# Optimization experiments

Hardware: AMD Instinct MI355X
Metric: run time of the kernel (lower is better)

The kernel has to match this reference:

```python
import jax, jax.numpy as jnp
import numpy as np

B, C, H, W = 64, 256, 32, 32
K, D = 1024, 256
COMMIT = 0.25
DECAY = 0.99
EPS = 1e-05


def setup_inputs() -> dict:
    key = jax.random.key(0)
    k1, k2, k3 = jax.random.split(key, 3)
    return {
        "inputs": jax.random.normal(k1, (B, C, H, W), dtype=jnp.float32),
        "embedding": jax.random.normal(k2, (K, D), dtype=jnp.float32),
        "ema_cluster_size": jnp.zeros((K,), dtype=jnp.float32),
        "ema_w": jax.random.normal(k3, (K, D), dtype=jnp.float32),
    }


def reference(inputs, embedding, ema_cluster_size, ema_w):
    # NCHW -> NHWC, flatten to [N, D]
    x = jnp.transpose(inputs, (0, 2, 3, 1))  # [B,H,W,D]
    in_shape = x.shape
    flat = x.reshape(-1, D)  # [N, D]

    dist = (jnp.sum(flat * flat, axis=1, keepdims=True)
            + jnp.sum(embedding * embedding, axis=1)
            - 2.0 * jnp.matmul(flat, embedding.T))
    idx = jnp.argmin(dist, axis=1)  # [N] int
    encodings = jax.nn.one_hot(idx, K, dtype=flat.dtype)  # [N, K]

    quantized = jnp.matmul(encodings, embedding).reshape(in_shape)  # [B,H,W,D]

    # EMA updates (training branch)
    cluster = ema_cluster_size * DECAY + (1.0 - DECAY) * jnp.sum(encodings, axis=0)
    n = jnp.sum(cluster)
    cluster = (cluster + EPS) / (n + K * EPS) * n
    dw = jnp.matmul(encodings.T, flat)  # [K, D]
    new_ema_w = ema_w * DECAY + (1.0 - DECAY) * dw
    new_embedding = new_ema_w / cluster[:, None]

    # commitment loss (quantized detached)
    e_latent_loss = jnp.mean((jax.lax.stop_gradient(quantized) - x) ** 2)
    loss = COMMIT * e_latent_loss

    # straight-through estimator
    quantized_st = x + jax.lax.stop_gradient(quantized - x)

    avg_probs = jnp.mean(encodings, axis=0)
    vq_entropy = -jnp.sum(avg_probs * jnp.log(avg_probs + 1e-10))

    out = jnp.transpose(quantized_st, (0, 3, 1, 2))  # back to NCHW
    return out, loss, vq_entropy, encodings, cluster, new_ema_w, new_embedding
```

## Files before the change

kernel.cpp:

```cpp
#include <hip/hip_runtime.h>

#define B_    64
#define C_    256
#define H_    32
#define W_    32
#define K_    1024
#define D_    256
#define HW_   1024
#define N_    65536
#define NELEM 16777216
#define DECAY_ 0.99f
#define OMD_   0.01f
#define EPS_   1e-5f
#define TAU_   0.05f

#define OFF_LOSS    16777216
#define OFF_ENT     16777217
#define OFF_ENC     16777218
#define OFF_CLUSTER 83886082
#define OFF_NEWW    83887106
#define OFF_NEWEMB  84149250

#define OFF_XHI     (OFF_ENC + 2)
#define OFF_XLO     (OFF_XHI + 8388608)
#define OFF_EHI     (OFF_XLO + 8388608)
#define OFF_ELO     (OFF_EHI + 131072)
#define OFF_SORT2   (OFF_ELO + 131072)
#define ZTAIL_ABS   33884168
#define ZTAIL_F4    12500478
#define ZHEAD_F4    4276737

typedef __attribute__((ext_vector_type(8)))  short short8;
typedef __attribute__((ext_vector_type(16))) float floatx16;

__device__ __forceinline__ unsigned short f2bf(float f) {
    unsigned u = __float_as_uint(f);
    return (unsigned short)((u + 0x7fffu + ((u >> 16) & 1u)) >> 16);
}
__device__ __forceinline__ float bf2f(unsigned short h) {
    return __uint_as_float(((unsigned)h) << 16);
}

__global__ __launch_bounds__(64) void k_prep_e(const float* __restrict__ emb,
                                               unsigned short* __restrict__ ehi,
                                               unsigned short* __restrict__ elo,
                                               float* __restrict__ enorm) {
    const int k = blockIdx.x;
    const int t = threadIdx.x;
    float4 v = ((const float4*)(emb + (size_t)k * D_))[t];
    float s = v.x * v.x + v.y * v.y + v.z * v.z + v.w * v.w;
    ushort4 hi, lo;
    {
        float f[4] = {v.x, v.y, v.z, v.w};
        unsigned short h[4], l[4];
        #pragma unroll
        for (int j = 0; j < 4; ++j) {
            h[j] = f2bf(f[j]);
            l[j] = f2bf(f[j] - bf2f(h[j]));
        }
        hi = make_ushort4(h[0], h[1], h[2], h[3]);
        lo = make_ushort4(l[0], l[1], l[2], l[3]);
    }
    size_t o = ((size_t)(k >> 5) << 13) + ((size_t)(t >> 2) << 9)
             + (((size_t)(t >> 1) & 1) << 8) + ((size_t)(k & 31) << 3) + ((t & 1) << 2);
    *(ushort4*)(ehi + o) = hi;
    *(ushort4*)(elo + o) = lo;
    #pragma unroll
    for (int off = 32; off > 0; off >>= 1) s += __shfl_down(s, off);
    if (t == 0) enorm[k] = s;
}

__global__ __launch_bounds__(256) void k_prep_x(const float* __restrict__ inp,
                                                unsigned short* __restrict__ xhi,
                                                unsigned short* __restrict__ xlo,
                                                float* __restrict__ dw,
                                                int* __restrict__ small_,
                                                int* __restrict__ cursor) {
    __shared__ float tile[32][257];
    const int tid = threadIdx.x;
    const int bid = blockIdx.x;
    if (bid < 1024) {
        int g = bid * 256 + tid;
        dw[g] = 0.0f;
        if (g < 1026) small_[g] = 0;
        if (bid < 4) cursor[bid * 256 + tid] = 0;
    }
    const int dt = bid & 7;
    const int ht = (bid >> 3) & 3;
    const int b = bid >> 5;
    const int d0 = dt * 32;
    const int hw0 = ht * 256;
    const float* src = inp + (size_t)b * (C_ * HW_) + (size_t)d0 * HW_ + hw0;
    #pragma unroll
    for (int i = 0; i < 8; ++i) {
        int idx4 = i * 256 + tid;
        int dl = idx4 >> 6;
        int nl4 = (idx4 & 63) * 4;
        float4 v = *(const float4*)(src + (size_t)dl * HW_ + nl4);
        tile[dl][nl4] = v.x; tile[dl][nl4 + 1] = v.y;
        tile[dl][nl4 + 2] = v.z; tile[dl][nl4 + 3] = v.w;
    }
    __syncthreads();
    const int nbase = b * HW_ + hw0;
    #pragma unroll
    for (int i = 0; i < 4; ++i) {
        int f8 = i * 256 + tid;
        int nl = f8 >> 2;
        int dpos = (f8 & 3) * 8;
        union { unsigned short u[8]; short8 v; } ph, pl;
        #pragma unroll
        for (int j = 0; j < 8; ++j) {
            float f = -2.0f * tile[dpos + j][nl];
            unsigned short h = f2bf(f);
            ph.u[j] = h;
            pl.u[j] = f2bf(f - bf2f(h));
        }
        size_t o = (size_t)(nbase + nl) * D_ + d0 + dpos;
        *(short8*)(xhi + o) = ph.v;
        *(short8*)(xlo + o) = pl.v;
    }
}

__device__ __forceinline__ void stage_tile(const unsigned short* __restrict__ gh,
                                           const unsigned short* __restrict__ gl,
                                           unsigned short* sh, unsigned short* sl,
                                           int tid) {
    #pragma unroll
    for (int i = 0; i < 4; ++i) {
        __builtin_amdgcn_global_load_lds(
            (const __attribute__((address_space(1))) unsigned int*)(gh + i * 2048 + tid * 8),
            (__attribute__((address_space(3))) unsigned int*)(sh + i * 2048 + tid * 8),
            16, 0, 0);
        __builtin_amdgcn_global_load_lds(
            (const __attribute__((address_space(1))) unsigned int*)(gl + i * 2048 + tid * 8),
            (__attribute__((address_space(3))) unsigned int*)(sl + i * 2048 + tid * 8),
            16, 0, 0);
    }
}

__global__ __launch_bounds__(256, 2) void k_argmin(
    const unsigned short* __restrict__ xhi, const unsigned short* __restrict__ xlo,
    const unsigned short* __restrict__ ehi, const unsigned short* __restrict__ elo,
    const float* __restrict__ enorm, int* __restrict__ idx_out,
    int* __restrict__ flagcount, int* __restrict__ flaglist,
    float4* __restrict__ encz, int* __restrict__ counts)
{
    __shared__ unsigned short smem[2][2][8192];
    const int tid = threadIdx.x;
    const int w = tid >> 6;
    const int lane = tid & 63;
    const int c32 = lane & 31;
    const int h = lane >> 5;
    const int r0 = blockIdx.x * 128 + w * 32;
    const int gtid = blockIdx.x * 256 + tid;
    const float4 z4 = make_float4(0.f, 0.f, 0.f, 0.f);

    short8 Ahi[16], Alo[16];
    {
        const unsigned short* pa = xhi + (size_t)(r0 + c32) * D_ + h * 8;
        const unsigned short* pl = xlo + (size_t)(r0 + c32) * D_ + h * 8;
        #pragma unroll
        for (int ds = 0; ds < 16; ++ds) {
            Ahi[ds] = *(const short8*)(pa + ds * 16);
            Alo[ds] = *(const short8*)(pl + ds * 16);
        }
    }

    float b1[16], b2[16];
    int bi[16];
    #pragma unroll
    for (int i = 0; i < 16; ++i) { b1[i] = 3.0e38f; b2[i] = 3.0e38f; bi[i] = 0; }

    stage_tile(ehi, elo, &smem[0][0][0], &smem[0][1][0], tid);
    __syncthreads();

    const int rb = (h << 8) + (c32 << 3);

    int cb = 0;
    for (int ct = 0; ct < 32; ++ct) {
        if (ct + 1 < 32) {
            stage_tile(ehi + (size_t)(ct + 1) * 8192, elo + (size_t)(ct + 1) * 8192,
                       &smem[cb ^ 1][0][0], &smem[cb ^ 1][1][0], tid);
        }
        __builtin_amdgcn_sched_barrier(0);
        #pragma unroll
        for (int jj = 0; jj < 3; ++jj) {
            int zi = (ct * 3 + jj) * 131072 + gtid;
            zi = (zi < ZTAIL_F4) ? zi : (ZTAIL_F4 - 1);
            encz[zi] = z4;
        }
        const int col = ct * 32 + c32;
        const float en = enorm[col];
        const unsigned short* sbh = &smem[cb][0][rb];
        const unsigned short* sbl = &smem[cb][1][rb];
        floatx16 hh, cr;
        #pragma unroll
        for (int i = 0; i < 16; ++i) { hh[i] = 0.0f; cr[i] = 0.0f; }
        #pragma unroll
        for (int ds = 0; ds < 16; ++ds) {
            short8 bh = *(const short8*)(sbh + ds * 512);
            short8 bl = *(const short8*)(sbl + ds * 512);
            hh = __builtin_amdgcn_mfma_f32_32x32x16_bf16(Ahi[ds], bh, hh, 0, 0, 0);
            cr = __builtin_amdgcn_mfma_f32_32x32x16_bf16(Ahi[ds], bl, cr, 0, 0, 0);
            cr = __builtin_amdgcn_mfma_f32_32x32x16_bf16(Alo[ds], bh, cr, 0, 0, 0);
        }
        #pragma unroll
        for (int r = 0; r < 16; ++r) {
            float v = hh[r] + cr[r] + en;
            bool lt = v < b1[r];
            float nb2 = lt ? b1[r] : fminf(v, b2[r]);
            b2[r] = nb2;
            b1[r] = lt ? v : b1[r];
            bi[r] = lt ? col : bi[r];
        }
        asm volatile("s_waitcnt vmcnt(3)" ::: "memory");
        __builtin_amdgcn_sched_barrier(0);
        __builtin_amdgcn_s_barrier();
        __builtin_amdgcn_sched_barrier(0);
        cb ^= 1;
    }

    int* histL = (int*)&smem[0][0][0];
    #pragma unroll
    for (int j = 0; j < 4; ++j) histL[tid + j * 256] = 0;
    __syncthreads();

    #pragma unroll
    for (int r = 0; r < 16; ++r) {
        float B1 = b1[r], B2 = b2[r];
        int Bi = bi[r];
        #pragma unroll
        for (int mask = 1; mask <= 16; mask <<= 1) {
            float v1 = __shfl_xor(B1, mask);
            float v2 = __shfl_xor(B2, mask);
            int i1 = __shfl_xor(Bi, mask);
            if (v1 < B1 || (v1 == B1 && i1 < Bi)) {
                B2 = fminf(fminf(B1, B2), v2);
                B1 = v1; Bi = i1;
            } else {
                B2 = fminf(B2, fminf(v1, v2));
            }
        }
        if (c32 == 0) {
            int row = r0 + (r & 3) + 4 * h + 8 * (r >> 2);
            idx_out[row] = Bi;
            atomicAdd(&histL[Bi], 1);
            if (B2 - B1 < TAU_) {
                int p = atomicAdd(flagcount, 1);
                flaglist[p] = row;
            }
        }
    }
    __syncthreads();
    #pragma unroll
    for (int j = 0; j < 4; ++j) {
        int v = histL[tid + j * 256];
        if (v) atomicAdd(&counts[tid + j * 256], v);
    }
}

__global__ __launch_bounds__(256) void k_rescan(
    const float* __restrict__ inp, const float* __restrict__ emb,
    const int* __restrict__ flagcount, const int* __restrict__ flaglist,
    int* __restrict__ idx_out, int* __restrict__ counts)
{
    __shared__ double xd[256];
    __shared__ double sv[256];
    __shared__ int si[256];
    const int tid = threadIdx.x;
    const int nflag = *flagcount;
    for (int f = blockIdx.x; f < nflag; f += gridDim.x) {
        int n = flaglist[f];
        int b = n >> 10, nn = n & 1023;
        xd[tid] = (double)inp[(size_t)b * (C_ * HW_) + (size_t)tid * HW_ + nn];
        __syncthreads();
        double bv = 1e300; int bi = 0;
        for (int k = tid; k < K_; k += 256) {
            const float* ep = emb + (size_t)k * D_;
            double dot = 0.0, en = 0.0;
            for (int d = 0; d < D_; ++d) {
                double e = (double)ep[d];
                dot = fma(xd[d], e, dot);
                en  = fma(e, e, en);
            }
            double v = en - 2.0 * dot;
            if (v < bv) { bv = v; bi = k; }
        }
        sv[tid] = bv; si[tid] = bi;
        __syncthreads();
        for (int s = 128; s > 0; s >>= 1) {
            if (tid < s) {
                if (sv[tid + s] < sv[tid] || (sv[tid + s] == sv[tid] && si[tid + s] < si[tid])) {
                    sv[tid] = sv[tid + s]; si[tid] = si[tid + s];
                }
            }
            __syncthreads();
        }
        if (tid == 0) {
            int old = idx_out[n];
            int nw = si[0];
            if (nw != old) {
                idx_out[n] = nw;
                atomicAdd(&counts[old], -1);
                atomicAdd(&counts[nw], 1);
            }
        }
        __syncthreads();
    }
}

__global__ __launch_bounds__(256) void k_scatter(const int* __restrict__ idx,
                                                 const int* __restrict__ counts,
                                                 int* __restrict__ cursor,
                                                 int* __restrict__ sorted,
                                                 int* __restrict__ offsets) {
    __shared__ int sc[1024];
    __shared__ int hc[1024];
    __shared__ int hb[1024];
    const int tid = threadIdx.x;
    const int base = blockIdx.x * 1024;
    int creg[4];
    #pragma unroll
    for (int j = 0; j < 4; ++j) {
        int k = tid + j * 256;
        creg[j] = counts[k];
        sc[k] = creg[j];
        hc[k] = 0;
    }
    __syncthreads();
    for (int off = 1; off < 1024; off <<= 1) {
        int t0[4];
        #pragma unroll
        for (int j = 0; j < 4; ++j) {
            int k = tid + j * 256;
            t0[j] = (k >= off) ? sc[k - off] : 0;
        }
        __syncthreads();
        #pragma unroll
        for (int j = 0; j < 4; ++j) sc[tid + j * 256] += t0[j];
        __syncthreads();
    }
    #pragma unroll
    for (int j = 0; j < 4; ++j) {
        int k = tid + j * 256;
        sc[k] -= creg[j];
    }
    __syncthreads();
    if (blockIdx.x == 0) {
        #pragma unroll
        for (int j = 0; j < 4; ++j) {
            int k = tid + j * 256;
            offsets[k] = sc[k];
            if (k == 1023) offsets[1024] = sc[1023] + creg[j];
        }
    }
    int myk[4], myn[4];
    #pragma unroll
    for (int j = 0; j < 4; ++j) {
        int n = base + j * 256 + tid;
        myn[j] = n;
        myk[j] = idx[n];
        atomicAdd(&hc[myk[j]], 1);
    }
    __syncthreads();
    #pragma unroll
    for (int j = 0; j < 4; ++j) {
        int kk = tid + j * 256;
        int c = hc[kk];
        hb[kk] = c ? atomicAdd(&cursor[kk], c) : 0;
    }
    __syncthreads();
    #pragma unroll
    for (int j = 0; j < 4; ++j) hc[tid + j * 256] = 0;
    __syncthreads();
    #pragma unroll
    for (int j = 0; j < 4; ++j) {
        int p = sc[myk[j]] + hb[myk[j]] + atomicAdd(&hc[myk[j]], 1);
        sorted[p] = myn[j];
    }
}

__global__ __launch_bounds__(256) void k_dwg(const unsigned short* __restrict__ xhi,
                                             const unsigned short* __restrict__ xlo,
                                             const int* __restrict__ sorted,
                                             const int* __restrict__ idx,
                                             const int* __restrict__ offsets,
                                             float* __restrict__ dw) {
    const int lane = threadIdx.x & 63;
    const int wid = threadIdx.x >> 6;
    const int wbase = (blockIdx.x * 4 + wid) * 64;

    int myn = sorted[wbase + lane];
    int myk = idx[myn];

    float4 acc = make_float4(0.f, 0.f, 0.f, 0.f);
    int cur = __shfl(myk, 0);

    #pragma unroll 8
    for (int i = 0; i < 64; ++i) {
        int n = __shfl(myn, i);
        int k = __shfl(myk, i);
        if (k != cur) {
            bool full = (offsets[cur] >= wbase) && (offsets[cur + 1] <= wbase + 64);
            float* dwk = dw + (size_t)cur * D_ + lane * 4;
            if (full) {
                ((float2*)dwk)[0] = make_float2(-0.5f * acc.x, -0.5f * acc.y);
                ((float2*)dwk)[1] = make_float2(-0.5f * acc.z, -0.5f * acc.w);
            } else {
                atomicAdd(dwk + 0, -0.5f * acc.x);
                atomicAdd(dwk + 1, -0.5f * acc.y);
                atomicAdd(dwk + 2, -0.5f * acc.z);
                atomicAdd(dwk + 3, -0.5f * acc.w);
            }
            acc = make_float4(0.f, 0.f, 0.f, 0.f);
            cur = k;
        }
        size_t o = (size_t)n * D_ + lane * 4;
        ushort4 hx = *(const ushort4*)(xhi + o);
        ushort4 lx = *(const ushort4*)(xlo + o);
        acc.x += bf2f(hx.x) + bf2f(lx.x);
        acc.y += bf2f(hx.y) + bf2f(lx.y);
        acc.z += bf2f(hx.z) + bf2f(lx.z);
        acc.w += bf2f(hx.w) + bf2f(lx.w);
    }
    {
        bool full = (offsets[cur] >= wbase) && (offsets[cur + 1] <= wbase + 64);
        float* dwk = dw + (size_t)cur * D_ + lane * 4;
        if (full) {
            ((float2*)dwk)[0] = make_float2(-0.5f * acc.x, -0.5f * acc.y);
            ((float2*)dwk)[1] = make_float2(-0.5f * acc.z, -0.5f * acc.w);
        } else {
            atomicAdd(dwk + 0, -0.5f * acc.x);
            atomicAdd(dwk + 1, -0.5f * acc.y);
            atomicAdd(dwk + 2, -0.5f * acc.z);
            atomicAdd(dwk + 3, -0.5f * acc.w);
        }
    }
}

__global__ __launch_bounds__(256) void k_quant(
    const float* __restrict__ inp, const float* __restrict__ emb,
    const int* __restrict__ idx, float* __restrict__ outp, float* __restrict__ losssum,
    float* __restrict__ enc)
{
    __shared__ float qt[64][260];
    __shared__ int karr[64];
    __shared__ float red[256];
    const int tid = threadIdx.x;
    const int bid = blockIdx.x;
    const int b = bid >> 4;
    const int ht = bid & 15;
    const int base_n = b * HW_ + ht * 64;

    {
        const float4 z4 = make_float4(0.f, 0.f, 0.f, 0.f);
        float4* pz = (float4*)(enc + 2);
        int t = bid * 256 + tid;
        #pragma unroll
        for (int it = 0; it < 17; ++it) {
            int i = it * 262144 + t;
            if (i < ZHEAD_F4) pz[i] = z4;
        }
        if (t == 0) { enc[0] = 0.f; enc[1] = 0.f; enc[67108862] = 0.f; enc[67108863] = 0.f; }
    }

    if (tid < 64) karr[tid] = idx[base_n + tid];
    __syncthreads();

    #pragma unroll
    for (int it = 0; it < 16; ++it) {
        int f = it * 256 + tid;
        int r = f >> 6;
        int c4 = (f & 63) << 2;
        float4 v = ((const float4*)emb)[karr[r] * 64 + (c4 >> 2)];
        *(float4*)(&qt[r][c4]) = v;
    }
    __syncthreads();

    float s = 0.0f;
    #pragma unroll
    for (int it = 0; it < 16; ++it) {
        int f = it * 256 + tid;
        int c = f >> 4;
        int hl = (f & 15) << 2;
        int g = b * 65536 + c * 256 + ht * 16 + (hl >> 2);
        float4 x = ((const float4*)inp)[g];
        float q0 = qt[hl + 0][c];
        float q1 = qt[hl + 1][c];
        float q2 = qt[hl + 2][c];
        float q3 = qt[hl + 3][c];
        float d0 = q0 - x.x, d1 = q1 - x.y, d2 = q2 - x.z, d3 = q3 - x.w;
        ((float4*)outp)[g] = make_float4(x.x + d0, x.y + d1, x.z + d2, x.w + d3);
        s += d0 * d0 + d1 * d1 + d2 * d2 + d3 * d3;
    }
    red[tid] = s;
    __syncthreads();
    for (int t = 128; t > 0; t >>= 1) {
        if (tid < t) red[tid] += red[tid + t];
        __syncthreads();
    }
    if (tid == 0) atomicAdd(losssum, red[0]);
}

__global__ __launch_bounds__(256) void k_fin(
    const float* __restrict__ ema_cs, const int* __restrict__ counts,
    const float* __restrict__ losssum, const float* __restrict__ ema_w,
    const int* __restrict__ idx,
    float* __restrict__ neww, float* __restrict__ newemb,
    float* __restrict__ out_cluster, float* __restrict__ out_loss,
    float* __restrict__ out_ent, float* __restrict__ enc)
{
    __shared__ float sraw[1024];
    __shared__ float red[256];
    __shared__ float sclv;
    const int tid = threadIdx.x;
    const int bid = blockIdx.x;
    float part = 0.f;
    float ent = 0.f;
    #pragma unroll
    for (int j = 0; j < 4; ++j) {
        int k = tid + j * 256;
        float cnt = (float)counts[k];
        float raw = ema_cs[k] * DECAY_ + OMD_ * cnt;
        sraw[k] = raw;
        part += raw;
        float p = cnt * (1.0f / 65536.0f);
        ent += p * logf(p + 1e-10f);
    }
    red[tid] = part;
    __syncthreads();
    for (int t = 128; t > 0; t >>= 1) {
        if (tid < t) red[tid] += red[tid + t];
        __syncthreads();
    }
    float nsum = red[0];
    __syncthreads();
    red[tid] = ent;
    __syncthreads();
    for (int t = 128; t > 0; t >>= 1) {
        if (tid < t) red[tid] += red[tid + t];
        __syncthreads();
    }
    if (tid == 0) {
        float clv = (sraw[bid] + EPS_) / (nsum + 1024.0f * EPS_) * nsum;
        sclv = clv;
        out_cluster[bid] = clv;
        if (bid == 0) {
            out_ent[0] = -red[0];
            out_loss[0] = 0.25f * losssum[0] * (1.0f / 16777216.0f);
        }
    }
    __syncthreads();
    float clv = sclv;
    int g = bid * 256 + tid;
    float w = ema_w[g] * DECAY_ + OMD_ * neww[g];
    neww[g] = w;
    newemb[g] = w / clv;
    if (tid < 64) {
        int n = bid * 64 + tid;
        enc[(size_t)n * 1024 + idx[n]] = 1.0f;
    }
}

extern "C" void kernel_launch(void* const* d_in, const int* in_sizes, int n_in,
                              void* d_out, int out_size, void* d_ws, size_t ws_size,
                              hipStream_t stream)
{
    const float* inp    = (const float*)d_in[0];
    const float* emb    = (const float*)d_in[1];
    const float* ema_cs = (const float*)d_in[2];
    const float* ema_w  = (const float*)d_in[3];

    float* out0        = (float*)d_out;
    float* out_loss    = out0 + OFF_LOSS;
    float* out_ent     = out0 + OFF_ENT;
    float* out_enc     = out0 + OFF_ENC;
    float* out_cluster = out0 + OFF_CLUSTER;
    float* out_neww    = out0 + OFF_NEWW;
    float* out_newemb  = out0 + OFF_NEWEMB;

    unsigned short* ws_xhi  = (unsigned short*)(out0 + OFF_XHI);
    unsigned short* ws_xlo  = (unsigned short*)(out0 + OFF_XLO);
    unsigned short* ws_ehi  = (unsigned short*)(out0 + OFF_EHI);
    unsigned short* ws_elo  = (unsigned short*)(out0 + OFF_ELO);
    int*   ws_sorted  = (int*)(out0 + OFF_SORT2);
    int*   ws_offsets = ws_sorted + 65536;
    int*   ws_cursor  = ws_offsets + 1025;

    int*   ws_idx    = (int*)d_ws;
    int*   ws_counts = ws_idx + 65536;
    int*   ws_flagc  = ws_idx + 66560;
    float* ws_loss   = (float*)(ws_idx + 66561);
    int*   ws_flagl  = ws_idx + 66562;
    float* ws_enorm  = (float*)(ws_idx + 132098);

    float4* encz = (float4*)(out0 + ZTAIL_ABS);

    k_prep_e <<<1024, 64, 0, stream>>>(emb, ws_ehi, ws_elo, ws_enorm);
    k_prep_x <<<2048, 256, 0, stream>>>(inp, ws_xhi, ws_xlo, out_neww, ws_counts, ws_cursor);
    k_argmin <<<512, 256, 0, stream>>>(ws_xhi, ws_xlo, ws_ehi, ws_elo, ws_enorm,
                                       ws_idx, ws_flagc, ws_flagl, encz, ws_counts);
    k_rescan <<<256, 256, 0, stream>>>(inp, emb, ws_flagc, ws_flagl, ws_idx, ws_counts);
    k_scatter<<<64, 256, 0, stream>>>(ws_idx, ws_counts, ws_cursor, ws_sorted, ws_offsets);
    k_dwg    <<<256, 256, 0, stream>>>(ws_xhi, ws_xlo, ws_sorted, ws_idx, ws_offsets, out_neww);
    k_quant  <<<1024, 256, 0, stream>>>(inp, emb, ws_idx, out0, ws_loss, out_enc);
    k_fin    <<<1024, 256, 0, stream>>>(ema_cs, ws_counts, ws_loss, ema_w, ws_idx,
                                        out_neww, out_newemb, out_cluster, out_loss,
                                        out_ent, out_enc);
}
```

Baseline: 651.6 us.

## Replace split-bf16 distance GEMM with split int8 fixed-point MFMA

Embeddings and inputs are quantized to 16-bit fixed point, split into hi/lo int8 halves, and the distance GEMM uses four i8 32x32x32 MFMAs per step instead of three bf16 MFMAs. This halves the workspace bytes and LDS traffic per tile and uses the higher int8 MFMA rate, and dw accumulation switches to integer sums. Fixed-point scaling with clamping loses range and precision for large values, which the near-tie rescan path must absorb. Workspace offsets and zero-fill loop counts are adjusted to the smaller buffers.

```diff
diff --git a/kernel.cpp b/kernel.cpp
--- a/kernel.cpp
+++ b/kernel.cpp
@@ -21,58 +21,51 @@
 #define OFF_NEWW    83887106
 #define OFF_NEWEMB  84149250
 
-#define OFF_XHI     (OFF_ENC + 2)
-#define OFF_XLO     (OFF_XHI + 8388608)
-#define OFF_EHI     (OFF_XLO + 8388608)
-#define OFF_ELO     (OFF_EHI + 131072)
-#define OFF_SORT2   (OFF_ELO + 131072)
-#define ZTAIL_ABS   33884168
-#define ZTAIL_F4    12500478
-#define ZHEAD_F4    4276737
+#define OFF_XH      (OFF_ENC + 2)
+#define OFF_XL      (OFF_XH + 4194304)
+#define OFF_EH      (OFF_XL + 4194304)
+#define OFF_EL      (OFF_EH + 65536)
+#define OFF_SORT2   (OFF_EL + 65536)
+#define ZTAIL_ABS   25364488
+#define ZTAIL_F4    14630398
+#define ZHEAD_F4    2146817
 
 typedef __attribute__((ext_vector_type(8)))  short short8;
-typedef __attribute__((ext_vector_type(16))) float floatx16;
-
-__device__ __forceinline__ unsigned short f2bf(float f) {
-    unsigned u = __float_as_uint(f);
-    return (unsigned short)((u + 0x7fffu + ((u >> 16) & 1u)) >> 16);
-}
-__device__ __forceinline__ float bf2f(unsigned short h) {
-    return __uint_as_float(((unsigned)h) << 16);
-}
+typedef __attribute__((ext_vector_type(4)))  int   intx4;
+typedef __attribute__((ext_vector_type(16))) int   intx16;
 
 __global__ __launch_bounds__(64) void k_prep_e(const float* __restrict__ emb,
-                                               unsigned short* __restrict__ ehi,
-                                               unsigned short* __restrict__ elo,
+                                               signed char* __restrict__ eh,
+                                               signed char* __restrict__ el,
                                                float* __restrict__ enorm) {
     const int k = blockIdx.x;
     const int t = threadIdx.x;
     float4 v = ((const float4*)(emb + (size_t)k * D_))[t];
     float s = v.x * v.x + v.y * v.y + v.z * v.z + v.w * v.w;
-    ushort4 hi, lo;
+    signed char hq[4], lq[4];
     {
         float f[4] = {v.x, v.y, v.z, v.w};
-        unsigned short h[4], l[4];
         #pragma unroll
         for (int j = 0; j < 4; ++j) {
-            h[j] = f2bf(f[j]);
-            l[j] = f2bf(f[j] - bf2f(h[j]));
-        }
-        hi = make_ushort4(h[0], h[1], h[2], h[3]);
-        lo = make_ushort4(l[0], l[1], l[2], l[3]);
-    }
-    size_t o = ((size_t)(k >> 5) << 13) + ((size_t)(t >> 2) << 9)
-             + (((size_t)(t >> 1) & 1) << 8) + ((size_t)(k & 31) << 3) + ((t & 1) << 2);
-    *(ushort4*)(ehi + o) = hi;
-    *(ushort4*)(elo + o) = lo;
+            int q = (int)rintf(f[j] * 2048.0f);
+            q = q < -32640 ? -32640 : (q > 32639 ? 32639 : q);
+            int hh = (q + 128) >> 8;
+            hq[j] = (signed char)hh;
+            lq[j] = (signed char)(q - (hh << 8));
+        }
+    }
+    size_t o = (size_t)(k >> 5) * 8192 + (size_t)(t >> 3) * 1024
+             + (size_t)((t >> 2) & 1) * 512 + (size_t)(k & 31) * 16 + (t & 3) * 4;
+    *(char4*)(eh + o) = make_char4(hq[0], hq[1], hq[2], hq[3]);
+    *(char4*)(el + o) = make_char4(lq[0], lq[1], lq[2], lq[3]);
     #pragma unroll
     for (int off = 32; off > 0; off >>= 1) s += __shfl_down(s, off);
     if (t == 0) enorm[k] = s;
 }
 
 __global__ __launch_bounds__(256) void k_prep_x(const float* __restrict__ inp,
-                                                unsigned short* __restrict__ xhi,
-                                                unsigned short* __restrict__ xlo,
+                                                signed char* __restrict__ xh,
+                                                signed char* __restrict__ xl,
                                                 float* __restrict__ dw,
                                                 int* __restrict__ small_,
                                                 int* __restrict__ cursor) {
@@ -107,45 +100,46 @@
         int f8 = i * 256 + tid;
         int nl = f8 >> 2;
         int dpos = (f8 & 3) * 8;
-        union { unsigned short u[8]; short8 v; } ph, pl;
+        union { signed char c[8]; long long v; } ph, pl;
         #pragma unroll
         for (int j = 0; j < 8; ++j) {
-            float f = -2.0f * tile[dpos + j][nl];
-            unsigned short h = f2bf(f);
-            ph.u[j] = h;
-            pl.u[j] = f2bf(f - bf2f(h));
+            int q = (int)rintf(-4096.0f * tile[dpos + j][nl]);
+            q = q < -32640 ? -32640 : (q > 32639 ? 32639 : q);
+            int hh = (q + 128) >> 8;
+            ph.c[j] = (signed char)hh;
+            pl.c[j] = (signed char)(q - (hh << 8));
         }
         size_t o = (size_t)(nbase + nl) * D_ + d0 + dpos;
-        *(short8*)(xhi + o) = ph.v;
-        *(short8*)(xlo + o) = pl.v;
-    }
-}
-
-__device__ __forceinline__ void stage_tile(const unsigned short* __restrict__ gh,
-                                           const unsigned short* __restrict__ gl,
-                                           unsigned short* sh, unsigned short* sl,
-                                           int tid) {
-    #pragma unroll
-    for (int i = 0; i < 4; ++i) {
+        *(long long*)(xh + o) = ph.v;
+        *(long long*)(xl + o) = pl.v;
+    }
+}
+
+__device__ __forceinline__ void stage_tile8(const signed char* __restrict__ gh,
+                                            const signed char* __restrict__ gl,
+                                            signed char* sh, signed char* sl,
+                                            int tid) {
+    #pragma unroll
+    for (int i = 0; i < 2; ++i) {
         __builtin_amdgcn_global_load_lds(
-            (const __attribute__((address_space(1))) unsigned int*)(gh + i * 2048 + tid * 8),
-            (__attribute__((address_space(3))) unsigned int*)(sh + i * 2048 + tid * 8),
+            (const __attribute__((address_space(1))) unsigned int*)(gh + i * 4096 + tid * 16),
+            (__attribute__((address_space(3))) unsigned int*)(sh + i * 4096 + tid * 16),
             16, 0, 0);
         __builtin_amdgcn_global_load_lds(
-            (const __attribute__((address_space(1))) unsigned int*)(gl + i * 2048 + tid * 8),
-            (__attribute__((address_space(3))) unsigned int*)(sl + i * 2048 + tid * 8),
+            (const __attribute__((address_space(1))) unsigned int*)(gl + i * 4096 + tid * 16),
+            (__attribute__((address_space(3))) unsigned int*)(sl + i * 4096 + tid * 16),
             16, 0, 0);
     }
 }
 
 __global__ __launch_bounds__(256, 2) void k_argmin(
-    const unsigned short* __restrict__ xhi, const unsigned short* __restrict__ xlo,
-    const unsigned short* __restrict__ ehi, const unsigned short* __restrict__ elo,
+    const signed char* __restrict__ xh, const signed char* __restrict__ xl,
+    const signed char* __restrict__ eh, const signed char* __restrict__ el,
     const float* __restrict__ enorm, int* __restrict__ idx_out,
     int* __restrict__ flagcount, int* __restrict__ flaglist,
     float4* __restrict__ encz, int* __restrict__ counts)
 {
-    __shared__ unsigned short smem[2][2][8192];
+    __shared__ __align__(16) signed char smem[2][2][8192];
     const int tid = threadIdx.x;
     const int w = tid >> 6;
     const int lane = tid & 63;
@@ -155,14 +149,14 @@
     const int gtid = blockIdx.x * 256 + tid;
     const float4 z4 = make_float4(0.f, 0.f, 0.f, 0.f);
 
-    short8 Ahi[16], Alo[16];
+    intx4 Ah[8], Al[8];
     {
-        const unsigned short* pa = xhi + (size_t)(r0 + c32) * D_ + h * 8;
-        const unsigned short* pl = xlo + (size_t)(r0 + c32) * D_ + h * 8;
-        #pragma unroll
-        for (int ds = 0; ds < 16; ++ds) {
-            Ahi[ds] = *(const short8*)(pa + ds * 16);
-            Alo[ds] = *(const short8*)(pl + ds * 16);
+        const signed char* pa = xh + (size_t)(r0 + c32) * D_ + h * 16;
+        const signed char* pl = xl + (size_t)(r0 + c32) * D_ + h * 16;
+        #pragma unroll
+        for (int ds = 0; ds < 8; ++ds) {
+            Ah[ds] = *(const intx4*)(pa + ds * 32);
+            Al[ds] = *(const intx4*)(pl + ds * 32);
         }
     }
 
@@ -171,49 +165,52 @@
     #pragma unroll
     for (int i = 0; i < 16; ++i) { b1[i] = 3.0e38f; b2[i] = 3.0e38f; bi[i] = 0; }
 
-    stage_tile(ehi, elo, &smem[0][0][0], &smem[0][1][0], tid);
-    __syncthreads();
-
-    const int rb = (h << 8) + (c32 << 3);
+    stage_tile8(eh, el, &smem[0][0][0], &smem[0][1][0], tid);
+    __syncthreads();
+
+    const int rb = (h << 9) + (c32 << 4);
 
     int cb = 0;
     for (int ct = 0; ct < 32; ++ct) {
         if (ct + 1 < 32) {
-            stage_tile(ehi + (size_t)(ct + 1) * 8192, elo + (size_t)(ct + 1) * 8192,
-                       &smem[cb ^ 1][0][0], &smem[cb ^ 1][1][0], tid);
+            stage_tile8(eh + (size_t)(ct + 1) * 8192, el + (size_t)(ct + 1) * 8192,
+                        &smem[cb ^ 1][0][0], &smem[cb ^ 1][1][0], tid);
         }
         __builtin_amdgcn_sched_barrier(0);
         #pragma unroll
-        for (int jj = 0; jj < 3; ++jj) {
-            int zi = (ct * 3 + jj) * 131072 + gtid;
+        for (int jj = 0; jj < 4; ++jj) {
+            int zi = (ct * 4 + jj) * 131072 + gtid;
             zi = (zi < ZTAIL_F4) ? zi : (ZTAIL_F4 - 1);
             encz[zi] = z4;
         }
         const int col = ct * 32 + c32;
         const float en = enorm[col];
-        const unsigned short* sbh = &smem[cb][0][rb];
-        const unsigned short* sbl = &smem[cb][1][rb];
-        floatx16 hh, cr;
-        #pragma unroll
-        for (int i = 0; i < 16; ++i) { hh[i] = 0.0f; cr[i] = 0.0f; }
-        #pragma unroll
-        for (int ds = 0; ds < 16; ++ds) {
-            short8 bh = *(const short8*)(sbh + ds * 512);
-            short8 bl = *(const short8*)(sbl + ds * 512);
-            hh = __builtin_amdgcn_mfma_f32_32x32x16_bf16(Ahi[ds], bh, hh, 0, 0, 0);
-            cr = __builtin_amdgcn_mfma_f32_32x32x16_bf16(Ahi[ds], bl, cr, 0, 0, 0);
-            cr = __builtin_amdgcn_mfma_f32_32x32x16_bf16(Alo[ds], bh, cr, 0, 0, 0);
+        const signed char* sbh = &smem[cb][0][rb];
+        const signed char* sbl = &smem[cb][1][rb];
+        intx16 hh, m1, m2, ll;
+        #pragma unroll
+        for (int i = 0; i < 16; ++i) { hh[i] = 0; m1[i] = 0; m2[i] = 0; ll[i] = 0; }
+        #pragma unroll
+        for (int ds = 0; ds < 8; ++ds) {
+            intx4 bh = *(const intx4*)(sbh + ds * 1024);
+            intx4 bl = *(const intx4*)(sbl + ds * 1024);
+            hh = __builtin_amdgcn_mfma_i32_32x32x32_i8(Ah[ds], bh, hh, 0, 0, 0);
+            m1 = __builtin_amdgcn_mfma_i32_32x32x32_i8(Ah[ds], bl, m1, 0, 0, 0);
+            m2 = __builtin_amdgcn_mfma_i32_32x32x32_i8(Al[ds], bh, m2, 0, 0, 0);
+            ll = __builtin_amdgcn_mfma_i32_32x32x32_i8(Al[ds], bl, ll, 0, 0, 0);
         }
         #pragma unroll
         for (int r = 0; r < 16; ++r) {
-            float v = hh[r] + cr[r] + en;
+            float dot = (float)hh[r] * 65536.0f + (float)(m1[r] + m2[r]) * 256.0f
+                      + (float)ll[r];
+            float v = en + dot * 2.384185791015625e-07f;
             bool lt = v < b1[r];
             float nb2 = lt ? b1[r] : fminf(v, b2[r]);
             b2[r] = nb2;
             b1[r] = lt ? v : b1[r];
             bi[r] = lt ? col : bi[r];
         }
-        asm volatile("s_waitcnt vmcnt(3)" ::: "memory");
+        asm volatile("s_waitcnt vmcnt(4)" ::: "memory");
         __builtin_amdgcn_sched_barrier(0);
         __builtin_amdgcn_s_barrier();
         __builtin_amdgcn_sched_barrier(0);
@@ -380,8 +377,8 @@
     }
 }
 
-__global__ __launch_bounds__(256) void k_dwg(const unsigned short* __restrict__ xhi,
-                                             const unsigned short* __restrict__ xlo,
+__global__ __launch_bounds__(256) void k_dwg(const signed char* __restrict__ xh,
+                                             const signed char* __restrict__ xl,
                                              const int* __restrict__ sorted,
                                              const int* __restrict__ idx,
                                              const int* __restrict__ offsets,
@@ -393,8 +390,9 @@
     int myn = sorted[wbase + lane];
     int myk = idx[myn];
 
-    float4 acc = make_float4(0.f, 0.f, 0.f, 0.f);
+    int4 acc = make_int4(0, 0, 0, 0);
     int cur = __shfl(myk, 0);
+    const float sc = -1.0f / 4096.0f;
 
     #pragma unroll 8
     for (int i = 0; i < 64; ++i) {
@@ -404,36 +402,36 @@
             bool full = (offsets[cur] >= wbase) && (offsets[cur + 1] <= wbase + 64);
             float* dwk = dw + (size_t)cur * D_ + lane * 4;
             if (full) {
-                ((float2*)dwk)[0] = make_float2(-0.5f * acc.x, -0.5f * acc.y);
-                ((float2*)dwk)[1] = make_float2(-0.5f * acc.z, -0.5f * acc.w);
+                ((float2*)dwk)[0] = make_float2(sc * acc.x, sc * acc.y);
+                ((float2*)dwk)[1] = make_float2(sc * acc.z, sc * acc.w);
             } else {
-                atomicAdd(dwk + 0, -0.5f * acc.x);
-                atomicAdd(dwk + 1, -0.5f * acc.y);
-                atomicAdd(dwk + 2, -0.5f * acc.z);
-                atomicAdd(dwk + 3, -0.5f * acc.w);
+                atomicAdd(dwk + 0, sc * acc.x);
+                atomicAdd(dwk + 1, sc * acc.y);
+                atomicAdd(dwk + 2, sc * acc.z);
+                atomicAdd(dwk + 3, sc * acc.w);
             }
-            acc = make_float4(0.f, 0.f, 0.f, 0.f);
+            acc = make_int4(0, 0, 0, 0);
             cur = k;
         }
         size_t o = (size_t)n * D_ + lane * 4;
-        ushort4 hx = *(const ushort4*)(xhi + o);
-        ushort4 lx = *(const ushort4*)(xlo + o);
-        acc.x += bf2f(hx.x) + bf2f(lx.x);
-        acc.y += bf2f(hx.y) + bf2f(lx.y);
-        acc.z += bf2f(hx.z) + bf2f(lx.z);
-        acc.w += bf2f(hx.w) + bf2f(lx.w);
+        char4 hx = *(const char4*)(xh + o);
+        char4 lx = *(const char4*)(xl + o);
+        acc.x += ((int)hx.x << 8) + (int)lx.x;
+        acc.y += ((int)hx.y << 8) + (int)lx.y;
+        acc.z += ((int)hx.z << 8) + (int)lx.z;
+        acc.w += ((int)hx.w << 8) + (int)lx.w;
     }
     {
         bool full = (offsets[cur] >= wbase) && (offsets[cur + 1] <= wbase + 64);
         float* dwk = dw + (size_t)cur * D_ + lane * 4;
         if (full) {
-            ((float2*)dwk)[0] = make_float2(-0.5f * acc.x, -0.5f * acc.y);
-            ((float2*)dwk)[1] = make_float2(-0.5f * acc.z, -0.5f * acc.w);
+            ((float2*)dwk)[0] = make_float2(sc * acc.x, sc * acc.y);
+            ((float2*)dwk)[1] = make_float2(sc * acc.z, sc * acc.w);
         } else {
-            atomicAdd(dwk + 0, -0.5f * acc.x);
-            atomicAdd(dwk + 1, -0.5f * acc.y);
-            atomicAdd(dwk + 2, -0.5f * acc.z);
-            atomicAdd(dwk + 3, -0.5f * acc.w);
+            atomicAdd(dwk + 0, sc * acc.x);
+            atomicAdd(dwk + 1, sc * acc.y);
+            atomicAdd(dwk + 2, sc * acc.z);
+            atomicAdd(dwk + 3, sc * acc.w);
         }
     }
 }
@@ -457,7 +455,7 @@
         float4* pz = (float4*)(enc + 2);
         int t = bid * 256 + tid;
         #pragma unroll
-        for (int it = 0; it < 17; ++it) {
+        for (int it = 0; it < 9; ++it) {
             int i = it * 262144 + t;
             if (i < ZHEAD_F4) pz[i] = z4;
         }
@@ -579,10 +577,10 @@
     float* out_neww    = out0 + OFF_NEWW;
     float* out_newemb  = out0 + OFF_NEWEMB;
 
-    unsigned short* ws_xhi  = (unsigned short*)(out0 + OFF_XHI);
-    unsigned short* ws_xlo  = (unsigned short*)(out0 + OFF_XLO);
-    unsigned short* ws_ehi  = (unsigned short*)(out0 + OFF_EHI);
-    unsigned short* ws_elo  = (unsigned short*)(out0 + OFF_ELO);
+    signed char* ws_xh = (signed char*)(out0 + OFF_XH);
+    signed char* ws_xl = (signed char*)(out0 + OFF_XL);
+    signed char* ws_eh = (signed char*)(out0 + OFF_EH);
+    signed char* ws_el = (signed char*)(out0 + OFF_EL);
     int*   ws_sorted  = (int*)(out0 + OFF_SORT2);
     int*   ws_offsets = ws_sorted + 65536;
     int*   ws_cursor  = ws_offsets + 1025;
@@ -596,13 +594,13 @@
 
     float4* encz = (float4*)(out0 + ZTAIL_ABS);
 
-    k_prep_e <<<1024, 64, 0, stream>>>(emb, ws_ehi, ws_elo, ws_enorm);
-    k_prep_x <<<2048, 256, 0, stream>>>(inp, ws_xhi, ws_xlo, out_neww, ws_counts, ws_cursor);
-    k_argmin <<<512, 256, 0, stream>>>(ws_xhi, ws_xlo, ws_ehi, ws_elo, ws_enorm,
+    k_prep_e <<<1024, 64, 0, stream>>>(emb, ws_eh, ws_el, ws_enorm);
+    k_prep_x <<<2048, 256, 0, stream>>>(inp, ws_xh, ws_xl, out_neww, ws_counts, ws_cursor);
+    k_argmin <<<512, 256, 0, stream>>>(ws_xh, ws_xl, ws_eh, ws_el, ws_enorm,
                                        ws_idx, ws_flagc, ws_flagl, encz, ws_counts);
     k_rescan <<<256, 256, 0, stream>>>(inp, emb, ws_flagc, ws_flagl, ws_idx, ws_counts);
     k_scatter<<<64, 256, 0, stream>>>(ws_idx, ws_counts, ws_cursor, ws_sorted, ws_offsets);
-    k_dwg    <<<256, 256, 0, stream>>>(ws_xhi, ws_xlo, ws_sorted, ws_idx, ws_offsets, out_neww);
+    k_dwg    <<<256, 256, 0, stream>>>(ws_xh, ws_xl, ws_sorted, ws_idx, ws_offsets, out_neww);
     k_quant  <<<1024, 256, 0, stream>>>(inp, emb, ws_idx, out0, ws_loss, out_enc);
     k_fin    <<<1024, 256, 0, stream>>>(ema_cs, ws_counts, ws_loss, ema_w, ws_idx,
                                         out_neww, out_newemb, out_cluster, out_loss,
```

Result: faster. 604.7 us (-7.2%).
